# Optimization experiments

Hardware: AMD Instinct MI355X
Metric: run time of the kernel (lower is better)

## Reference

```python
import jax, jax.numpy as jnp
import numpy as np

N_GENE = 4762
N_CELL = 847


def _graph_conv(x_src, src, dst, n_src, n_dst, W, b):
    """DGL GraphConv with norm='both': D_src^{-1/2} A D_dst^{-1/2} X W + b."""
    ones_e = jnp.ones(src.shape, jnp.float32)
    deg_out = jax.ops.segment_sum(ones_e, src, num_segments=n_src)
    norm_src = jnp.clip(deg_out, 1.0, None) ** -0.5
    feat = x_src * norm_src[:, None]            # [n_src, d]
    msg = feat[src]                              # gather  [E, d]
    agg = jax.ops.segment_sum(msg, dst, num_segments=n_dst)  # scatter-add [n_dst, d]
    deg_in = jax.ops.segment_sum(ones_e, dst, num_segments=n_dst)
    norm_dst = jnp.clip(deg_in, 1.0, None) ** -0.5
    return (agg * norm_dst[:, None]) @ W + b


def setup_inputs() -> dict:
    key = jax.random.key(0)
    ks = jax.random.split(key, 12)
    E = 200000
    d = 256
    inp = {
        "gene_emb": jax.random.normal(ks[0], (N_GENE, d), jnp.float32),
        "cell_emb": jax.random.normal(ks[1], (N_CELL, d), jnp.float32),
        "W_g2c": jax.random.normal(ks[2], (d, d), jnp.float32) * (1.0 / np.sqrt(d)),
        "b_g2c": jnp.zeros((d,), jnp.float32),
        "W_c2g": jax.random.normal(ks[3], (d, d), jnp.float32) * (1.0 / np.sqrt(d)),
        "b_c2g": jnp.zeros((d,), jnp.float32),
        "Wp": jax.random.normal(ks[4], (2 * d, 1), jnp.float32) * (1.0 / np.sqrt(2 * d)),
        "bp": jnp.zeros((1,), jnp.float32),
        "g2c_src": jax.random.randint(ks[5], (E,), 0, N_GENE, jnp.int32),
        "g2c_dst": jax.random.randint(ks[6], (E,), 0, N_CELL, jnp.int32),
        "c2g_src": jax.random.randint(ks[7], (E,), 0, N_CELL, jnp.int32),
        "c2g_dst": jax.random.randint(ks[8], (E,), 0, N_GENE, jnp.int32),
        "dec_src": jax.random.randint(ks[9], (E,), 0, N_GENE, jnp.int32),
        "dec_dst": jax.random.randint(ks[10], (E,), 0, N_CELL, jnp.int32),
    }
    return inp


def reference(gene_emb, cell_emb, W_g2c, b_g2c, W_c2g, b_c2g, Wp, bp,
              g2c_src, g2c_dst, c2g_src, c2g_dst, dec_src, dec_dst):
    # HeteroGraphConv (aggregate='sum'): each dst type receives from one relation here.
    h_cell = _graph_conv(gene_emb, g2c_src, g2c_dst, N_GENE, N_CELL, W_g2c, b_g2c)
    h_gene = _graph_conv(cell_emb, c2g_src, c2g_dst, N_CELL, N_GENE, W_c2g, b_c2g)
    h_gene = jax.nn.relu(h_gene)
    h_cell = jax.nn.relu(h_cell)
    # HeteroMLPPredictor: concat(src_h, dst_h) @ Wp + bp on dec_graph edges.
    x = jnp.concatenate([h_gene[dec_src], h_cell[dec_dst]], axis=1)  # [E_dec, 512]
    score = x @ Wp + bp                                               # [E_dec, 1]
    return (score, h_gene, h_cell)
```

## Files before the change

### kernel.cpp

```cpp
#include <hip/hip_runtime.h>

#define N_GENE 4762
#define N_CELL 847
#define NEDGE  200000
#define D      256
#define NPART  64

typedef __attribute__((ext_vector_type(8))) short short8;
typedef __attribute__((ext_vector_type(8))) unsigned short ushort8v;
typedef __attribute__((ext_vector_type(4))) float f32x4;

#define S_G_OUT 0
#define S_C_IN  (S_G_OUT + N_GENE)
#define S_C_OUT (S_C_IN + N_CELL)
#define S_G_IN  (S_C_OUT + N_CELL)
#define NBINS   (S_G_IN + N_GENE)

#define ALIGN8(x) (((x) + 7) & ~7)

#define A_DEG      0
#define A_NRM      (A_DEG + NBINS)
#define A_OFFS_C   (A_NRM + NBINS)
#define A_OFFS_G   (A_OFFS_C + N_CELL + 1)
#define A_SORT_C   ALIGN8(A_OFFS_G + N_GENE + 1)
#define A_SORT_G   (A_SORT_C + 2 * NEDGE)
#define A_PART     (A_SORT_G + 2 * NEDGE)
#define A_SG       (A_PART + NPART * NBINS)
#define A_SC       (A_SG + N_GENE)
#define A_GENE_BF  ALIGN8(A_SC + N_CELL)
#define A_CELL_BF  ALIGN8(A_GENE_BF + N_GENE * D / 2)
#define A_WT1_BF   ALIGN8(A_CELL_BF + N_CELL * D / 2)
#define A_WT2_BF   ALIGN8(A_WT1_BF + D * D / 2)
#define A_AGGC_BF  ALIGN8(A_WT2_BF + D * D / 2)
#define A_AGGG_BF  ALIGN8(A_AGGC_BF + N_CELL * D / 2)

__device__ __forceinline__ unsigned short f2bf(float f) {
    unsigned u = __float_as_uint(f);
    u = (u + 0x7FFFu + ((u >> 16) & 1u)) >> 16;
    return (unsigned short)u;
}
__device__ __forceinline__ float bf2f(unsigned short b) {
    return __uint_as_float(((unsigned)b) << 16);
}

__global__ __launch_bounds__(1024) void k_pre(
        const int* __restrict__ g2c_src, const int* __restrict__ g2c_dst,
        const int* __restrict__ c2g_src, const int* __restrict__ c2g_dst,
        const float* __restrict__ gene_emb, const float* __restrict__ cell_emb,
        const float* __restrict__ W_g2c, const float* __restrict__ W_c2g,
        int* __restrict__ partial,
        unsigned short* __restrict__ gene_bf, unsigned short* __restrict__ cell_bf,
        unsigned short* __restrict__ wt1, unsigned short* __restrict__ wt2,
        float* __restrict__ sg, float* __restrict__ sc) {
    __shared__ int sh[N_GENE];
    int B = blockIdx.x, T = threadIdx.x;
    if (B < 4 * NPART) {
        int grp = B >> 6, blk = B & (NPART - 1);
        const int* idx;
        int segbase, segn;
        if      (grp == 0) { idx = g2c_src; segbase = S_G_OUT; segn = N_GENE; }
        else if (grp == 1) { idx = g2c_dst; segbase = S_C_IN;  segn = N_CELL; }
        else if (grp == 2) { idx = c2g_src; segbase = S_C_OUT; segn = N_CELL; }
        else               { idx = c2g_dst; segbase = S_G_IN;  segn = N_GENE; }
        for (int j = T; j < segn; j += 1024) sh[j] = 0;
        __syncthreads();
        const int chunk = (NEDGE + NPART - 1) / NPART;
        int e0 = blk * chunk, e1 = min(NEDGE, e0 + chunk);
        for (int e = e0 + T; e < e1; e += 1024) atomicAdd(&sh[idx[e]], 1);
        __syncthreads();
        int* pp = partial + blk * NBINS + segbase;
        for (int j = T; j < segn; j += 1024) pp[j] = sh[j];
    } else {
        const int NG = N_GENE * D, NC = N_CELL * D, NW = D * D;
        int base = (B - 4 * NPART) * 1024 + T;
        const int CH = (NG + NC) / 8;
        for (int c = base; c < CH; c += 64 * 1024) {
            const float* sp;
            unsigned short* dp;
            if (c < NG / 8) { sp = gene_emb + c * 8; dp = gene_bf + c * 8; }
            else { int j = (c - NG / 8) * 8; sp = cell_emb + j; dp = cell_bf + j; }
            f32x4 x0 = *(const f32x4*)sp;
            f32x4 x1 = *(const f32x4*)(sp + 4);
            ushort8v o;
            o[0] = f2bf(x0[0]); o[1] = f2bf(x0[1]);
            o[2] = f2bf(x0[2]); o[3] = f2bf(x0[3]);
            o[4] = f2bf(x1[0]); o[5] = f2bf(x1[1]);
            o[6] = f2bf(x1[2]); o[7] = f2bf(x1[3]);
            *(ushort8v*)dp = o;
        }
        for (int i = base; i < 2 * NW; i += 64 * 1024) {
            if (i < NW) {
                wt1[i] = f2bf(W_g2c[(i & 255) * D + (i >> 8)]);
            } else {
                int j = i - NW;
                wt2[j] = f2bf(W_c2g[(j & 255) * D + (j >> 8)]);
            }
        }
        for (int i = base; i < N_GENE + N_CELL; i += 64 * 1024) {
            if (i < N_GENE) sg[i] = 0.f; else sc[i - N_GENE] = 0.f;
        }
    }
}

__global__ void k_reduce(int* __restrict__ partial, int* __restrict__ deg,
                         float* __restrict__ nrm) {
    int j = blockIdx.x * blockDim.x + threadIdx.x;
    if (j < NBINS) {
        int s = 0;
        #pragma unroll
        for (int b0 = 0; b0 < NPART; b0 += 32) {
            int t[32];
            #pragma unroll
            for (int u = 0; u < 32; u++) t[u] = partial[(b0 + u) * NBINS + j];
            #pragma unroll
            for (int u = 0; u < 32; u++) { partial[(b0 + u) * NBINS + j] = s; s += t[u]; }
        }
        deg[j] = s;
        nrm[j] = rsqrtf(fmaxf((float)s, 1.0f));
    }
}

__global__ __launch_bounds__(1024) void k_scatter(
        const int* __restrict__ g2c_src, const int* __restrict__ g2c_dst,
        const int* __restrict__ c2g_src, const int* __restrict__ c2g_dst,
        const int* __restrict__ deg, const int* __restrict__ partial,
        const float* __restrict__ nrm,
        int* __restrict__ offsC, int* __restrict__ offsG,
        int2* __restrict__ sortC, int2* __restrict__ sortG) {
    __shared__ int soffs[N_GENE + 1];
    __shared__ int scur[N_GENE];
    __shared__ int wsum[16];
    int T = threadIdx.x, blk = blockIdx.x, dir = blockIdx.y;
    const int* src  = dir ? c2g_src : g2c_src;
    const int* dst  = dir ? c2g_dst : g2c_dst;
    const int* dgs  = dir ? deg + S_G_IN : deg + S_C_IN;
    const float* nsv = dir ? nrm + S_C_OUT : nrm + S_G_OUT;
    int seg         = dir ? S_G_IN : S_C_IN;
    int nb          = dir ? N_GENE : N_CELL;
    int* goffs      = dir ? offsG : offsC;
    int2* sorted    = dir ? sortG : sortC;
    int per = (nb + 1023) >> 10;
    int i0 = T * per, i1 = min(nb, i0 + per);
    int loc[5];
    int s = 0;
    for (int i = i0; i < i1; i++) { loc[i - i0] = s; s += dgs[i]; }
    int lane = T & 63, w = T >> 6;
    int t = s;
    #pragma unroll
    for (int off = 1; off < 64; off <<= 1) {
        int u = __shfl_up(t, off);
        if (lane >= off) t += u;
    }
    if (lane == 63) wsum[w] = t;
    __syncthreads();
    if (w == 0 && lane < 16) {
        int x = wsum[lane];
        #pragma unroll
        for (int off = 1; off < 16; off <<= 1) {
            int u = __shfl_up(x, off);
            if (lane >= off) x += u;
        }
        wsum[lane] = x;
    }
    __syncthreads();
    int wbase = w ? wsum[w - 1] : 0;
    int excl = wbase + t - s;
    for (int i = i0; i < i1; i++) soffs[i] = excl + loc[i - i0];
    if (T == 1023) soffs[nb] = excl + s;
    __syncthreads();
    if (blk == 0)
        for (int j = T; j <= nb; j += 1024) goffs[j] = soffs[j];
    const int* basep = partial + blk * NBINS + seg;
    for (int j = T; j < nb; j += 1024) scur[j] = soffs[j] + basep[j];
    __syncthreads();
    const int chunk = (NEDGE + NPART - 1) / NPART;
    int e0 = blk * chunk, e1 = min(NEDGE, e0 + chunk);
    for (int e = e0 + T; e < e1; e += 1024) {
        int d = dst[e], sv = src[e];
        float nv = nsv[sv];
        int pos = atomicAdd(&scur[d], 1);
        sorted[pos] = make_int2(sv, __float_as_int(nv));
    }
}

__global__ __launch_bounds__(256) void k_agg(
        const unsigned short* __restrict__ gene_bf,
        const unsigned short* __restrict__ cell_bf,
        const int2* __restrict__ sortC, const int2* __restrict__ sortG,
        const int* __restrict__ offsC, const int* __restrict__ offsG,
        const float* __restrict__ nrm,
        unsigned short* __restrict__ aggC, unsigned short* __restrict__ aggG) {
    __shared__ int   sidx[4][64];
    __shared__ float snrm[4][64];
    const int CB = (N_CELL + 3) / 4;
    int w = threadIdx.x >> 6, lane = threadIdx.x & 63;
    int half = lane >> 5, li = lane & 31;
    int B = blockIdx.x;
    bool isCell = B < CB;

    int e0, e1, node;
    const unsigned short* emb;
    const int2* sorted;
    unsigned short* outp;
    int nseg;
    if (isCell) {
        node = B * 4 + w;
        if (node >= N_CELL) return;
        e0 = offsC[node]; e1 = offsC[node + 1];
        emb = gene_bf; sorted = sortC; outp = aggC; nseg = S_C_IN;
    } else {
        node = (B - CB) * 4 + w;
        if (node >= N_GENE) return;
        e0 = offsG[node]; e1 = offsG[node + 1];
        emb = cell_bf; sorted = sortG; outp = aggG; nseg = S_G_IN;
    }

    float acc[8];
    #pragma unroll
    for (int c = 0; c < 8; c++) acc[c] = 0.f;

    for (int base = e0; base < e1; base += 64) {
        int n = min(64, e1 - base);
        if (lane < n) {
            int2 pr = sorted[base + lane];
            sidx[w][lane] = pr.x;
            snrm[w][lane] = __int_as_float(pr.y);
        }
        int i = 0;
        for (; 2 * i + 32 <= n; i += 16) {
            ushort8v v[16];
            float nv[16];
            #pragma unroll
            for (int k = 0; k < 16; k++) {
                int jj = 2 * (i + k) + half;
                v[k] = *(const ushort8v*)&emb[sidx[w][jj] * D + li * 8];
                nv[k] = snrm[w][jj];
            }
            #pragma unroll
            for (int c = 0; c < 8; c++) {
                float s0 = 0.f;
                #pragma unroll
                for (int k = 0; k < 16; k++) s0 += bf2f(v[k][c]) * nv[k];
                acc[c] += s0;
            }
        }
        for (; 2 * i + 16 <= n; i += 8) {
            ushort8v v[8];
            float nv[8];
            #pragma unroll
            for (int k = 0; k < 8; k++) {
                int jj = 2 * (i + k) + half;
                v[k] = *(const ushort8v*)&emb[sidx[w][jj] * D + li * 8];
                nv[k] = snrm[w][jj];
            }
            #pragma unroll
            for (int c = 0; c < 8; c++) {
                float s0 = 0.f;
                #pragma unroll
                for (int k = 0; k < 8; k++) s0 += bf2f(v[k][c]) * nv[k];
                acc[c] += s0;
            }
        }
        for (; 2 * i + 8 <= n; i += 4) {
            int j0 = 2 * i + half, j1 = 2 * i + 2 + half;
            int j2 = 2 * i + 4 + half, j3 = 2 * i + 6 + half;
            ushort8v v0 = *(const ushort8v*)&emb[sidx[w][j0] * D + li * 8];
            ushort8v v1 = *(const ushort8v*)&emb[sidx[w][j1] * D + li * 8];
            ushort8v v2 = *(const ushort8v*)&emb[sidx[w][j2] * D + li * 8];
            ushort8v v3 = *(const ushort8v*)&emb[sidx[w][j3] * D + li * 8];
            float n0 = snrm[w][j0], n1 = snrm[w][j1];
            float n2 = snrm[w][j2], n3 = snrm[w][j3];
            #pragma unroll
            for (int c = 0; c < 8; c++)
                acc[c] += bf2f(v0[c]) * n0 + bf2f(v1[c]) * n1 +
                          bf2f(v2[c]) * n2 + bf2f(v3[c]) * n3;
        }
        int npair = (n + 1) >> 1;
        for (; i < npair; i++) {
            int jj = 2 * i + half;
            bool ok = jj < n;
            int idx = ok ? sidx[w][jj] : sidx[w][0];
            float nv = ok ? snrm[w][jj] : 0.f;
            ushort8v v = *(const ushort8v*)&emb[idx * D + li * 8];
            #pragma unroll
            for (int c = 0; c < 8; c++) acc[c] += bf2f(v[c]) * nv;
        }
    }
    #pragma unroll
    for (int c = 0; c < 8; c++) acc[c] += __shfl_xor(acc[c], 32);

    if (half == 0) {
        float ndv = nrm[nseg + node];
        ushort8v o;
        #pragma unroll
        for (int c = 0; c < 8; c++) o[c] = f2bf(acc[c] * ndv);
        *(ushort8v*)&outp[node * D + li * 8] = o;
    }
}

__global__ __launch_bounds__(256) void k_gemm2(
        const unsigned short* __restrict__ aggC, const unsigned short* __restrict__ aggG,
        const unsigned short* __restrict__ wt1, const unsigned short* __restrict__ wt2,
        const float* __restrict__ b_g2c, const float* __restrict__ b_c2g,
        const float* __restrict__ Wp,
        float* __restrict__ hC, float* __restrict__ hG,
        float* __restrict__ sg, float* __restrict__ sc) {
    const int CT = (N_CELL + 15) / 16;
    const int GT = (N_GENE + 15) / 16;
    int wid = blockIdx.x * 4 + (threadIdx.x >> 6);
    if (wid >= (CT + GT) * 4) return;
    int tid = wid >> 2, nq = wid & 3;
    int n0 = nq * 64;
    bool isCell = tid < CT;
    int tile = isCell ? tid : tid - CT;
    int m0 = tile * 16;
    int M = isCell ? N_CELL : N_GENE;
    const unsigned short* A  = isCell ? aggC : aggG;
    const unsigned short* Wt = isCell ? wt1 : wt2;
    const float* bias = isCell ? b_g2c : b_c2g;
    const float* wp   = isCell ? Wp + D : Wp;
    float* H  = isCell ? hC : hG;
    float* sv = isCell ? sc : sg;
    int lane = threadIdx.x & 63;
    int l15 = lane & 15, quad = lane >> 4;
    int arow = m0 + l15;
    if (arow >= M) arow = M - 1;
    f32x4 acc[4];
    #pragma unroll
    for (int t = 0; t < 4; t++) acc[t] = (f32x4){0.f, 0.f, 0.f, 0.f};
    #pragma unroll
    for (int k0 = 0; k0 < D; k0 += 32) {
        short8 a = *(const short8*)&A[arow * D + k0 + quad * 8];
        #pragma unroll
        for (int t = 0; t < 4; t++) {
            short8 b = *(const short8*)&Wt[(n0 + t * 16 + l15) * D + k0 + quad * 8];
            acc[t] = __builtin_amdgcn_mfma_f32_16x16x32_bf16(a, b, acc[t], 0, 0, 0);
        }
    }
    float dot[4] = {0.f, 0.f, 0.f, 0.f};
    #pragma unroll
    for (int t = 0; t < 4; t++) {
        int col = n0 + t * 16 + l15;
        float bv = bias[col], wv = wp[col];
        #pragma unroll
        for (int r = 0; r < 4; r++) {
            int row = m0 + quad * 4 + r;
            float h = fmaxf(acc[t][r] + bv, 0.f);
            if (row < M) H[row * D + col] = h;
            dot[r] += h * wv;
        }
    }
    #pragma unroll
    for (int off = 1; off < 16; off <<= 1) {
        #pragma unroll
        for (int r = 0; r < 4; r++) dot[r] += __shfl_xor(dot[r], off);
    }
    if (l15 == 0) {
        #pragma unroll
        for (int r = 0; r < 4; r++) {
            int row = m0 + quad * 4 + r;
            if (row < M) atomicAdd(&sv[row], dot[r]);
        }
    }
}

__global__ void k_score(const int* __restrict__ dsrc, const int* __restrict__ ddst,
                        const float* __restrict__ sg, const float* __restrict__ sc,
                        const float* __restrict__ bp, float* __restrict__ out) {
    int i = blockIdx.x * blockDim.x + threadIdx.x;
    if (i < NEDGE) out[i] = sg[dsrc[i]] + sc[ddst[i]] + bp[0];
}

extern "C" void kernel_launch(void* const* d_in, const int* in_sizes, int n_in,
                              void* d_out, int out_size, void* d_ws, size_t ws_size,
                              hipStream_t stream) {
    const float* gene_emb = (const float*)d_in[0];
    const float* cell_emb = (const float*)d_in[1];
    const float* W_g2c    = (const float*)d_in[2];
    const float* b_g2c    = (const float*)d_in[3];
    const float* W_c2g    = (const float*)d_in[4];
    const float* b_c2g    = (const float*)d_in[5];
    const float* Wp       = (const float*)d_in[6];
    const float* bp       = (const float*)d_in[7];
    const int* g2c_src = (const int*)d_in[8];
    const int* g2c_dst = (const int*)d_in[9];
    const int* c2g_src = (const int*)d_in[10];
    const int* c2g_dst = (const int*)d_in[11];
    const int* dec_src = (const int*)d_in[12];
    const int* dec_dst = (const int*)d_in[13];

    int*   wsi = (int*)d_ws;
    float* wsf = (float*)d_ws;
    unsigned short* gene_bf = (unsigned short*)(wsi + A_GENE_BF);
    unsigned short* cell_bf = (unsigned short*)(wsi + A_CELL_BF);
    unsigned short* wt1     = (unsigned short*)(wsi + A_WT1_BF);
    unsigned short* wt2     = (unsigned short*)(wsi + A_WT2_BF);
    unsigned short* aggC    = (unsigned short*)(wsi + A_AGGC_BF);
    unsigned short* aggG    = (unsigned short*)(wsi + A_AGGG_BF);
    int2* sortC = (int2*)(wsi + A_SORT_C);
    int2* sortG = (int2*)(wsi + A_SORT_G);

    float* out = (float*)d_out;
    float* out_score = out;
    float* out_hgene = out + NEDGE;
    float* out_hcell = out + NEDGE + N_GENE * D;

    k_pre<<<4 * NPART + 64, 1024, 0, stream>>>(g2c_src, g2c_dst, c2g_src, c2g_dst,
                                               gene_emb, cell_emb, W_g2c, W_c2g,
                                               wsi + A_PART, gene_bf, cell_bf, wt1, wt2,
                                               wsf + A_SG, wsf + A_SC);
    k_reduce<<<(NBINS + 255) / 256, 256, 0, stream>>>(wsi + A_PART, wsi + A_DEG,
                                                      wsf + A_NRM);
    {
        dim3 grid(NPART, 2);
        k_scatter<<<grid, 1024, 0, stream>>>(g2c_src, g2c_dst, c2g_src, c2g_dst,
                                             wsi + A_DEG, wsi + A_PART, wsf + A_NRM,
                                             wsi + A_OFFS_C, wsi + A_OFFS_G,
                                             sortC, sortG);
    }
    {
        const int CB = (N_CELL + 3) / 4, GB = (N_GENE + 3) / 4;
        k_agg<<<CB + GB, 256, 0, stream>>>(
            gene_bf, cell_bf, sortC, sortG, wsi + A_OFFS_C, wsi + A_OFFS_G,
            wsf + A_NRM, aggC, aggG);
    }
    {
        const int CT = (N_CELL + 15) / 16, GT = (N_GENE + 15) / 16;
        k_gemm2<<<CT + GT, 256, 0, stream>>>(aggC, aggG, wt1, wt2,
                                             b_g2c, b_c2g, Wp,
                                             out_hcell, out_hgene,
                                             wsf + A_SG, wsf + A_SC);
    }
    k_score<<<(NEDGE + 255) / 256, 256, 0, stream>>>(dec_src, dec_dst,
                                                     wsf + A_SG, wsf + A_SC, bp, out_score);
}
```

Baseline: 141.4 us.

## Split cell aggregation into fixed edge chunks with atomic fp32 accumulation

Cell-destination aggregation used one wave per cell. With about 236 edges per cell that gave few, long waves, so the work was poorly balanced. It now splits the sorted edge list into 128-edge chunks, one per wave. Each wave binary-searches the CSR offsets to find its starting cell and atomically adds partial sums into an fp32 buffer, which k_pre zeroes. The aggregate buffers become fp32, and the destination-norm scaling plus bf16 conversion move into the GEMM's A-load. This adds atomic traffic and doubles the size of the intermediate buffers.

```diff
diff --git a/kernel.cpp b/kernel.cpp
--- a/kernel.cpp
+++ b/kernel.cpp
@@ -5,6 +5,7 @@
 #define NEDGE  200000
 #define D      256
 #define NPART  64
+#define CCHUNK 128
 
 typedef __attribute__((ext_vector_type(8))) short short8;
 typedef __attribute__((ext_vector_type(8))) unsigned short ushort8v;
@@ -31,8 +32,8 @@
 #define A_CELL_BF  ALIGN8(A_GENE_BF + N_GENE * D / 2)
 #define A_WT1_BF   ALIGN8(A_CELL_BF + N_CELL * D / 2)
 #define A_WT2_BF   ALIGN8(A_WT1_BF + D * D / 2)
-#define A_AGGC_BF  ALIGN8(A_WT2_BF + D * D / 2)
-#define A_AGGG_BF  ALIGN8(A_AGGC_BF + N_CELL * D / 2)
+#define A_AGGC_F   ALIGN8(A_WT2_BF + D * D / 2)
+#define A_AGGG_F   (A_AGGC_F + N_CELL * D)
 
 __device__ __forceinline__ unsigned short f2bf(float f) {
     unsigned u = __float_as_uint(f);
@@ -51,7 +52,8 @@
         int* __restrict__ partial,
         unsigned short* __restrict__ gene_bf, unsigned short* __restrict__ cell_bf,
         unsigned short* __restrict__ wt1, unsigned short* __restrict__ wt2,
-        float* __restrict__ sg, float* __restrict__ sc) {
+        float* __restrict__ sg, float* __restrict__ sc,
+        float* __restrict__ aggCf) {
     __shared__ int sh[N_GENE];
     int B = blockIdx.x, T = threadIdx.x;
     if (B < 4 * NPART) {
@@ -99,6 +101,9 @@
         for (int i = base; i < N_GENE + N_CELL; i += 64 * 1024) {
             if (i < N_GENE) sg[i] = 0.f; else sc[i - N_GENE] = 0.f;
         }
+        f32x4 z = {0.f, 0.f, 0.f, 0.f};
+        for (int i = base; i < N_CELL * D / 4; i += 64 * 1024)
+            ((f32x4*)aggCf)[i] = z;
     }
 }
 
@@ -183,126 +188,149 @@
     }
 }
 
+__device__ __forceinline__ void gather_acc(
+        const unsigned short* __restrict__ emb,
+        const int2* __restrict__ sorted,
+        int* __restrict__ sidxw, float* __restrict__ snrmw,
+        int lane, int half, int li, int rs, int re, float acc[8]) {
+    for (int base = rs; base < re; base += 64) {
+        int n = min(64, re - base);
+        if (lane < n) {
+            int2 pr = sorted[base + lane];
+            sidxw[lane] = pr.x;
+            snrmw[lane] = __int_as_float(pr.y);
+        }
+        int i = 0;
+        for (; 2 * i + 32 <= n; i += 16) {
+            ushort8v v[16];
+            float nv[16];
+            #pragma unroll
+            for (int k = 0; k < 16; k++) {
+                int jj = 2 * (i + k) + half;
+                v[k] = *(const ushort8v*)&emb[sidxw[jj] * D + li * 8];
+                nv[k] = snrmw[jj];
+            }
+            #pragma unroll
+            for (int c = 0; c < 8; c++) {
+                float s0 = 0.f;
+                #pragma unroll
+                for (int k = 0; k < 16; k++) s0 += bf2f(v[k][c]) * nv[k];
+                acc[c] += s0;
+            }
+        }
+        for (; 2 * i + 16 <= n; i += 8) {
+            ushort8v v[8];
+            float nv[8];
+            #pragma unroll
+            for (int k = 0; k < 8; k++) {
+                int jj = 2 * (i + k) + half;
+                v[k] = *(const ushort8v*)&emb[sidxw[jj] * D + li * 8];
+                nv[k] = snrmw[jj];
+            }
+            #pragma unroll
+            for (int c = 0; c < 8; c++) {
+                float s0 = 0.f;
+                #pragma unroll
+                for (int k = 0; k < 8; k++) s0 += bf2f(v[k][c]) * nv[k];
+                acc[c] += s0;
+            }
+        }
+        for (; 2 * i + 8 <= n; i += 4) {
+            int j0 = 2 * i + half, j1 = 2 * i + 2 + half;
+            int j2 = 2 * i + 4 + half, j3 = 2 * i + 6 + half;
+            ushort8v v0 = *(const ushort8v*)&emb[sidxw[j0] * D + li * 8];
+            ushort8v v1 = *(const ushort8v*)&emb[sidxw[j1] * D + li * 8];
+            ushort8v v2 = *(const ushort8v*)&emb[sidxw[j2] * D + li * 8];
+            ushort8v v3 = *(const ushort8v*)&emb[sidxw[j3] * D + li * 8];
+            float n0 = snrmw[j0], n1 = snrmw[j1];
+            float n2 = snrmw[j2], n3 = snrmw[j3];
+            #pragma unroll
+            for (int c = 0; c < 8; c++)
+                acc[c] += bf2f(v0[c]) * n0 + bf2f(v1[c]) * n1 +
+                          bf2f(v2[c]) * n2 + bf2f(v3[c]) * n3;
+        }
+        int npair = (n + 1) >> 1;
+        for (; i < npair; i++) {
+            int jj = 2 * i + half;
+            bool ok = jj < n;
+            int idx = ok ? sidxw[jj] : sidxw[0];
+            float nv = ok ? snrmw[jj] : 0.f;
+            ushort8v v = *(const ushort8v*)&emb[idx * D + li * 8];
+            #pragma unroll
+            for (int c = 0; c < 8; c++) acc[c] += bf2f(v[c]) * nv;
+        }
+    }
+}
+
 __global__ __launch_bounds__(256) void k_agg(
         const unsigned short* __restrict__ gene_bf,
         const unsigned short* __restrict__ cell_bf,
         const int2* __restrict__ sortC, const int2* __restrict__ sortG,
         const int* __restrict__ offsC, const int* __restrict__ offsG,
-        const float* __restrict__ nrm,
-        unsigned short* __restrict__ aggC, unsigned short* __restrict__ aggG) {
+        float* __restrict__ aggCf, float* __restrict__ aggGf) {
     __shared__ int   sidx[4][64];
     __shared__ float snrm[4][64];
-    const int CB = (N_CELL + 3) / 4;
+    const int NCH  = (NEDGE + CCHUNK - 1) / CCHUNK;
+    const int CBLK = (NCH + 3) / 4;
     int w = threadIdx.x >> 6, lane = threadIdx.x & 63;
     int half = lane >> 5, li = lane & 31;
     int B = blockIdx.x;
-    bool isCell = B < CB;
-
-    int e0, e1, node;
-    const unsigned short* emb;
-    const int2* sorted;
-    unsigned short* outp;
-    int nseg;
-    if (isCell) {
-        node = B * 4 + w;
-        if (node >= N_CELL) return;
-        e0 = offsC[node]; e1 = offsC[node + 1];
-        emb = gene_bf; sorted = sortC; outp = aggC; nseg = S_C_IN;
+
+    if (B < CBLK) {
+        int chunk = B * 4 + w;
+        if (chunk >= NCH) return;
+        int e0 = chunk * CCHUNK, e1 = min(NEDGE, e0 + CCHUNK);
+        int lo = 0, hi = N_CELL - 1;
+        while (lo < hi) {
+            int m = (lo + hi + 1) >> 1;
+            if (offsC[m] <= e0) lo = m; else hi = m - 1;
+        }
+        int d = lo, rs = e0;
+        while (rs < e1 && d < N_CELL) {
+            int re = min(e1, offsC[d + 1]);
+            if (re > rs) {
+                float acc[8];
+                #pragma unroll
+                for (int c = 0; c < 8; c++) acc[c] = 0.f;
+                gather_acc(gene_bf, sortC, sidx[w], snrm[w],
+                           lane, half, li, rs, re, acc);
+                #pragma unroll
+                for (int c = 0; c < 8; c++) acc[c] += __shfl_xor(acc[c], 32);
+                if (half == 0) {
+                    float* dstp = &aggCf[d * D + li * 8];
+                    #pragma unroll
+                    for (int c = 0; c < 8; c++) atomicAdd(&dstp[c], acc[c]);
+                }
+                rs = re;
+            }
+            d++;
+        }
     } else {
-        node = (B - CB) * 4 + w;
+        int node = (B - CBLK) * 4 + w;
         if (node >= N_GENE) return;
-        e0 = offsG[node]; e1 = offsG[node + 1];
-        emb = cell_bf; sorted = sortG; outp = aggG; nseg = S_G_IN;
-    }
-
-    float acc[8];
-    #pragma unroll
-    for (int c = 0; c < 8; c++) acc[c] = 0.f;
-
-    for (int base = e0; base < e1; base += 64) {
-        int n = min(64, e1 - base);
-        if (lane < n) {
-            int2 pr = sorted[base + lane];
-            sidx[w][lane] = pr.x;
-            snrm[w][lane] = __int_as_float(pr.y);
-        }
-        int i = 0;
-        for (; 2 * i + 32 <= n; i += 16) {
-            ushort8v v[16];
-            float nv[16];
-            #pragma unroll
-            for (int k = 0; k < 16; k++) {
-                int jj = 2 * (i + k) + half;
-                v[k] = *(const ushort8v*)&emb[sidx[w][jj] * D + li * 8];
-                nv[k] = snrm[w][jj];
-            }
-            #pragma unroll
-            for (int c = 0; c < 8; c++) {
-                float s0 = 0.f;
-                #pragma unroll
-                for (int k = 0; k < 16; k++) s0 += bf2f(v[k][c]) * nv[k];
-                acc[c] += s0;
-            }
-        }
-        for (; 2 * i + 16 <= n; i += 8) {
-            ushort8v v[8];
-            float nv[8];
-            #pragma unroll
-            for (int k = 0; k < 8; k++) {
-                int jj = 2 * (i + k) + half;
-                v[k] = *(const ushort8v*)&emb[sidx[w][jj] * D + li * 8];
-                nv[k] = snrm[w][jj];
-            }
-            #pragma unroll
-            for (int c = 0; c < 8; c++) {
-                float s0 = 0.f;
-                #pragma unroll
-                for (int k = 0; k < 8; k++) s0 += bf2f(v[k][c]) * nv[k];
-                acc[c] += s0;
-            }
-        }
-        for (; 2 * i + 8 <= n; i += 4) {
-            int j0 = 2 * i + half, j1 = 2 * i + 2 + half;
-            int j2 = 2 * i + 4 + half, j3 = 2 * i + 6 + half;
-            ushort8v v0 = *(const ushort8v*)&emb[sidx[w][j0] * D + li * 8];
-            ushort8v v1 = *(const ushort8v*)&emb[sidx[w][j1] * D + li * 8];
-            ushort8v v2 = *(const ushort8v*)&emb[sidx[w][j2] * D + li * 8];
-            ushort8v v3 = *(const ushort8v*)&emb[sidx[w][j3] * D + li * 8];
-            float n0 = snrm[w][j0], n1 = snrm[w][j1];
-            float n2 = snrm[w][j2], n3 = snrm[w][j3];
-            #pragma unroll
-            for (int c = 0; c < 8; c++)
-                acc[c] += bf2f(v0[c]) * n0 + bf2f(v1[c]) * n1 +
-                          bf2f(v2[c]) * n2 + bf2f(v3[c]) * n3;
-        }
-        int npair = (n + 1) >> 1;
-        for (; i < npair; i++) {
-            int jj = 2 * i + half;
-            bool ok = jj < n;
-            int idx = ok ? sidx[w][jj] : sidx[w][0];
-            float nv = ok ? snrm[w][jj] : 0.f;
-            ushort8v v = *(const ushort8v*)&emb[idx * D + li * 8];
-            #pragma unroll
-            for (int c = 0; c < 8; c++) acc[c] += bf2f(v[c]) * nv;
-        }
-    }
-    #pragma unroll
-    for (int c = 0; c < 8; c++) acc[c] += __shfl_xor(acc[c], 32);
-
-    if (half == 0) {
-        float ndv = nrm[nseg + node];
-        ushort8v o;
-        #pragma unroll
-        for (int c = 0; c < 8; c++) o[c] = f2bf(acc[c] * ndv);
-        *(ushort8v*)&outp[node * D + li * 8] = o;
+        int e0 = offsG[node], e1 = offsG[node + 1];
+        float acc[8];
+        #pragma unroll
+        for (int c = 0; c < 8; c++) acc[c] = 0.f;
+        gather_acc(cell_bf, sortG, sidx[w], snrm[w],
+                   lane, half, li, e0, e1, acc);
+        #pragma unroll
+        for (int c = 0; c < 8; c++) acc[c] += __shfl_xor(acc[c], 32);
+        if (half == 0) {
+            f32x4 o0, o1;
+            #pragma unroll
+            for (int c = 0; c < 4; c++) { o0[c] = acc[c]; o1[c] = acc[4 + c]; }
+            *(f32x4*)&aggGf[node * D + li * 8] = o0;
+            *(f32x4*)&aggGf[node * D + li * 8 + 4] = o1;
+        }
     }
 }
 
 __global__ __launch_bounds__(256) void k_gemm2(
-        const unsigned short* __restrict__ aggC, const unsigned short* __restrict__ aggG,
+        const float* __restrict__ aggCf, const float* __restrict__ aggGf,
         const unsigned short* __restrict__ wt1, const unsigned short* __restrict__ wt2,
         const float* __restrict__ b_g2c, const float* __restrict__ b_c2g,
-        const float* __restrict__ Wp,
+        const float* __restrict__ Wp, const float* __restrict__ nrm,
         float* __restrict__ hC, float* __restrict__ hG,
         float* __restrict__ sg, float* __restrict__ sc) {
     const int CT = (N_CELL + 15) / 16;
@@ -315,22 +343,31 @@
     int tile = isCell ? tid : tid - CT;
     int m0 = tile * 16;
     int M = isCell ? N_CELL : N_GENE;
-    const unsigned short* A  = isCell ? aggC : aggG;
+    const float* A = isCell ? aggCf : aggGf;
     const unsigned short* Wt = isCell ? wt1 : wt2;
     const float* bias = isCell ? b_g2c : b_c2g;
     const float* wp   = isCell ? Wp + D : Wp;
     float* H  = isCell ? hC : hG;
     float* sv = isCell ? sc : sg;
+    int nseg  = isCell ? S_C_IN : S_G_IN;
     int lane = threadIdx.x & 63;
     int l15 = lane & 15, quad = lane >> 4;
     int arow = m0 + l15;
     if (arow >= M) arow = M - 1;
+    float nrmv = nrm[nseg + arow];
     f32x4 acc[4];
     #pragma unroll
     for (int t = 0; t < 4; t++) acc[t] = (f32x4){0.f, 0.f, 0.f, 0.f};
     #pragma unroll
     for (int k0 = 0; k0 < D; k0 += 32) {
-        short8 a = *(const short8*)&A[arow * D + k0 + quad * 8];
+        f32x4 a0 = *(const f32x4*)&A[arow * D + k0 + quad * 8];
+        f32x4 a1 = *(const f32x4*)&A[arow * D + k0 + quad * 8 + 4];
+        short8 a;
+        #pragma unroll
+        for (int j = 0; j < 4; j++) {
+            a[j]     = (short)f2bf(a0[j] * nrmv);
+            a[4 + j] = (short)f2bf(a1[j] * nrmv);
+        }
         #pragma unroll
         for (int t = 0; t < 4; t++) {
             short8 b = *(const short8*)&Wt[(n0 + t * 16 + l15) * D + k0 + quad * 8];
@@ -395,8 +432,8 @@
     unsigned short* cell_bf = (unsigned short*)(wsi + A_CELL_BF);
     unsigned short* wt1     = (unsigned short*)(wsi + A_WT1_BF);
     unsigned short* wt2     = (unsigned short*)(wsi + A_WT2_BF);
-    unsigned short* aggC    = (unsigned short*)(wsi + A_AGGC_BF);
-    unsigned short* aggG    = (unsigned short*)(wsi + A_AGGG_BF);
+    float* aggCf = wsf + A_AGGC_F;
+    float* aggGf = wsf + A_AGGG_F;
     int2* sortC = (int2*)(wsi + A_SORT_C);
     int2* sortG = (int2*)(wsi + A_SORT_G);
 
@@ -408,7 +445,7 @@
     k_pre<<<4 * NPART + 64, 1024, 0, stream>>>(g2c_src, g2c_dst, c2g_src, c2g_dst,
                                                gene_emb, cell_emb, W_g2c, W_c2g,
                                                wsi + A_PART, gene_bf, cell_bf, wt1, wt2,
-                                               wsf + A_SG, wsf + A_SC);
+                                               wsf + A_SG, wsf + A_SC, aggCf);
     k_reduce<<<(NBINS + 255) / 256, 256, 0, stream>>>(wsi + A_PART, wsi + A_DEG,
                                                       wsf + A_NRM);
     {
@@ -419,15 +456,16 @@
                                              sortC, sortG);
     }
     {
-        const int CB = (N_CELL + 3) / 4, GB = (N_GENE + 3) / 4;
-        k_agg<<<CB + GB, 256, 0, stream>>>(
+        const int NCH = (NEDGE + CCHUNK - 1) / CCHUNK;
+        const int CBLK = (NCH + 3) / 4, GB = (N_GENE + 3) / 4;
+        k_agg<<<CBLK + GB, 256, 0, stream>>>(
             gene_bf, cell_bf, sortC, sortG, wsi + A_OFFS_C, wsi + A_OFFS_G,
-            wsf + A_NRM, aggC, aggG);
+            aggCf, aggGf);
     }
     {
         const int CT = (N_CELL + 15) / 16, GT = (N_GENE + 15) / 16;
-        k_gemm2<<<CT + GT, 256, 0, stream>>>(aggC, aggG, wt1, wt2,
-                                             b_g2c, b_c2g, Wp,
+        k_gemm2<<<CT + GT, 256, 0, stream>>>(aggCf, aggGf, wt1, wt2,
+                                             b_g2c, b_c2g, Wp, wsf + A_NRM,
                                              out_hcell, out_hgene,
                                              wsf + A_SG, wsf + A_SC);
     }
```

Measured after the change: 147.4 us. 1.04x slower.

## Fuse front-end and back-end kernels with inter-block flag synchronization

Applied to the files above, without the earlier changes.

Merges the histogram, prefix-reduce and scatter kernels into one launch, and the GEMM and score kernels into another. Dependent block groups spin-wait on per-block flags in workspace, set with release and acquire fences. This removes three kernel launches and their gaps. The flags are never reset, so on repeated calls they already hold the magic value and the waits fall through, which can race with stale data. The scheme also relies on producer blocks being resident before consumers spin.

```diff
diff --git a/kernel.cpp b/kernel.cpp
--- a/kernel.cpp
+++ b/kernel.cpp
@@ -5,6 +5,7 @@
 #define NEDGE  200000
 #define D      256
 #define NPART  64
+#define MAGIC  0x7A3B9C1D
 
 typedef __attribute__((ext_vector_type(8))) short short8;
 typedef __attribute__((ext_vector_type(8))) unsigned short ushort8v;
@@ -27,7 +28,8 @@
 #define A_PART     (A_SORT_G + 2 * NEDGE)
 #define A_SG       (A_PART + NPART * NBINS)
 #define A_SC       (A_SG + N_GENE)
-#define A_GENE_BF  ALIGN8(A_SC + N_CELL)
+#define A_FLAGS    ALIGN8(A_SC + N_CELL)
+#define A_GENE_BF  ALIGN8(A_FLAGS + 640)
 #define A_CELL_BF  ALIGN8(A_GENE_BF + N_GENE * D / 2)
 #define A_WT1_BF   ALIGN8(A_CELL_BF + N_CELL * D / 2)
 #define A_WT2_BF   ALIGN8(A_WT1_BF + D * D / 2)
@@ -43,17 +45,38 @@
     return __uint_as_float(((unsigned)b) << 16);
 }
 
-__global__ __launch_bounds__(1024) void k_pre(
+__device__ __forceinline__ void sig(int* slot) {
+    __builtin_amdgcn_fence(__ATOMIC_RELEASE, "agent");
+    __hip_atomic_store(slot, MAGIC, __ATOMIC_RELAXED, __HIP_MEMORY_SCOPE_AGENT);
+}
+__device__ __forceinline__ void waitflags(const int* slots, int n, int T, int nthr) {
+    for (int s = T; s < n; s += nthr) {
+        long long t0 = (long long)__builtin_amdgcn_s_memrealtime();
+        while (__hip_atomic_load(&slots[s], __ATOMIC_RELAXED,
+                                 __HIP_MEMORY_SCOPE_AGENT) != MAGIC) {
+            __builtin_amdgcn_s_sleep(2);
+            if ((long long)__builtin_amdgcn_s_memrealtime() - t0 > 50000000LL) break;
+        }
+    }
+    __syncthreads();
+    __builtin_amdgcn_fence(__ATOMIC_ACQUIRE, "agent");
+}
+
+__global__ __launch_bounds__(1024) void k_front(
         const int* __restrict__ g2c_src, const int* __restrict__ g2c_dst,
         const int* __restrict__ c2g_src, const int* __restrict__ c2g_dst,
         const float* __restrict__ gene_emb, const float* __restrict__ cell_emb,
         const float* __restrict__ W_g2c, const float* __restrict__ W_c2g,
-        int* __restrict__ partial,
+        int* __restrict__ partial, int* __restrict__ deg, float* __restrict__ nrm,
+        int* __restrict__ offsC, int* __restrict__ offsG,
+        int2* __restrict__ sortC, int2* __restrict__ sortG,
         unsigned short* __restrict__ gene_bf, unsigned short* __restrict__ cell_bf,
         unsigned short* __restrict__ wt1, unsigned short* __restrict__ wt2,
-        float* __restrict__ sg, float* __restrict__ sc) {
-    __shared__ int sh[N_GENE];
+        float* __restrict__ sg, float* __restrict__ sc,
+        int* __restrict__ flags) {
+    __shared__ int shm[2 * N_GENE + 24];
     int B = blockIdx.x, T = threadIdx.x;
+
     if (B < 4 * NPART) {
         int grp = B >> 6, blk = B & (NPART - 1);
         const int* idx;
@@ -62,15 +85,17 @@
         else if (grp == 1) { idx = g2c_dst; segbase = S_C_IN;  segn = N_CELL; }
         else if (grp == 2) { idx = c2g_src; segbase = S_C_OUT; segn = N_CELL; }
         else               { idx = c2g_dst; segbase = S_G_IN;  segn = N_GENE; }
-        for (int j = T; j < segn; j += 1024) sh[j] = 0;
+        for (int j = T; j < segn; j += 1024) shm[j] = 0;
         __syncthreads();
         const int chunk = (NEDGE + NPART - 1) / NPART;
         int e0 = blk * chunk, e1 = min(NEDGE, e0 + chunk);
-        for (int e = e0 + T; e < e1; e += 1024) atomicAdd(&sh[idx[e]], 1);
+        for (int e = e0 + T; e < e1; e += 1024) atomicAdd(&shm[idx[e]], 1);
         __syncthreads();
         int* pp = partial + blk * NBINS + segbase;
-        for (int j = T; j < segn; j += 1024) pp[j] = sh[j];
-    } else {
+        for (int j = T; j < segn; j += 1024) pp[j] = shm[j];
+        __syncthreads();
+        if (T == 0) sig(&flags[B]);
+    } else if (B < 4 * NPART + 64) {
         const int NG = N_GENE * D, NC = N_CELL * D, NW = D * D;
         int base = (B - 4 * NPART) * 1024 + T;
         const int CH = (NG + NC) / 8;
@@ -99,87 +124,81 @@
         for (int i = base; i < N_GENE + N_CELL; i += 64 * 1024) {
             if (i < N_GENE) sg[i] = 0.f; else sc[i - N_GENE] = 0.f;
         }
-    }
-}
-
-__global__ void k_reduce(int* __restrict__ partial, int* __restrict__ deg,
-                         float* __restrict__ nrm) {
-    int j = blockIdx.x * blockDim.x + threadIdx.x;
-    if (j < NBINS) {
+    } else if (B < 4 * NPART + 64 + 11) {
+        waitflags(flags, 256, T, 1024);
+        int j = (B - (4 * NPART + 64)) * 1024 + T;
+        if (j < NBINS) {
+            int s = 0;
+            #pragma unroll
+            for (int b0 = 0; b0 < NPART; b0 += 32) {
+                int t[32];
+                #pragma unroll
+                for (int u = 0; u < 32; u++) t[u] = partial[(b0 + u) * NBINS + j];
+                #pragma unroll
+                for (int u = 0; u < 32; u++) { partial[(b0 + u) * NBINS + j] = s; s += t[u]; }
+            }
+            deg[j] = s;
+            nrm[j] = rsqrtf(fmaxf((float)s, 1.0f));
+        }
+        __syncthreads();
+        if (T == 0) sig(&flags[256 + (B - (4 * NPART + 64))]);
+    } else {
+        waitflags(flags + 256, 11, T, 1024);
+        int idx2 = B - (4 * NPART + 64 + 11);
+        int blk = idx2 & (NPART - 1), dir = idx2 >> 6;
+        int* soffs = shm;
+        int* scur  = shm + N_GENE + 1;
+        int* wsum  = shm + 2 * N_GENE + 1;
+        const int* src  = dir ? c2g_src : g2c_src;
+        const int* dst  = dir ? c2g_dst : g2c_dst;
+        const int* dgs  = dir ? deg + S_G_IN : deg + S_C_IN;
+        const float* nsv = dir ? nrm + S_C_OUT : nrm + S_G_OUT;
+        int seg         = dir ? S_G_IN : S_C_IN;
+        int nb          = dir ? N_GENE : N_CELL;
+        int* goffs      = dir ? offsG : offsC;
+        int2* sorted    = dir ? sortG : sortC;
+        int per = (nb + 1023) >> 10;
+        int i0 = T * per, i1 = min(nb, i0 + per);
+        int loc[5];
         int s = 0;
-        #pragma unroll
-        for (int b0 = 0; b0 < NPART; b0 += 32) {
-            int t[32];
-            #pragma unroll
-            for (int u = 0; u < 32; u++) t[u] = partial[(b0 + u) * NBINS + j];
-            #pragma unroll
-            for (int u = 0; u < 32; u++) { partial[(b0 + u) * NBINS + j] = s; s += t[u]; }
-        }
-        deg[j] = s;
-        nrm[j] = rsqrtf(fmaxf((float)s, 1.0f));
-    }
-}
-
-__global__ __launch_bounds__(1024) void k_scatter(
-        const int* __restrict__ g2c_src, const int* __restrict__ g2c_dst,
-        const int* __restrict__ c2g_src, const int* __restrict__ c2g_dst,
-        const int* __restrict__ deg, const int* __restrict__ partial,
-        const float* __restrict__ nrm,
-        int* __restrict__ offsC, int* __restrict__ offsG,
-        int2* __restrict__ sortC, int2* __restrict__ sortG) {
-    __shared__ int soffs[N_GENE + 1];
-    __shared__ int scur[N_GENE];
-    __shared__ int wsum[16];
-    int T = threadIdx.x, blk = blockIdx.x, dir = blockIdx.y;
-    const int* src  = dir ? c2g_src : g2c_src;
-    const int* dst  = dir ? c2g_dst : g2c_dst;
-    const int* dgs  = dir ? deg + S_G_IN : deg + S_C_IN;
-    const float* nsv = dir ? nrm + S_C_OUT : nrm + S_G_OUT;
-    int seg         = dir ? S_G_IN : S_C_IN;
-    int nb          = dir ? N_GENE : N_CELL;
-    int* goffs      = dir ? offsG : offsC;
-    int2* sorted    = dir ? sortG : sortC;
-    int per = (nb + 1023) >> 10;
-    int i0 = T * per, i1 = min(nb, i0 + per);
-    int loc[5];
-    int s = 0;
-    for (int i = i0; i < i1; i++) { loc[i - i0] = s; s += dgs[i]; }
-    int lane = T & 63, w = T >> 6;
-    int t = s;
-    #pragma unroll
-    for (int off = 1; off < 64; off <<= 1) {
-        int u = __shfl_up(t, off);
-        if (lane >= off) t += u;
-    }
-    if (lane == 63) wsum[w] = t;
-    __syncthreads();
-    if (w == 0 && lane < 16) {
-        int x = wsum[lane];
-        #pragma unroll
-        for (int off = 1; off < 16; off <<= 1) {
-            int u = __shfl_up(x, off);
-            if (lane >= off) x += u;
-        }
-        wsum[lane] = x;
-    }
-    __syncthreads();
-    int wbase = w ? wsum[w - 1] : 0;
-    int excl = wbase + t - s;
-    for (int i = i0; i < i1; i++) soffs[i] = excl + loc[i - i0];
-    if (T == 1023) soffs[nb] = excl + s;
-    __syncthreads();
-    if (blk == 0)
-        for (int j = T; j <= nb; j += 1024) goffs[j] = soffs[j];
-    const int* basep = partial + blk * NBINS + seg;
-    for (int j = T; j < nb; j += 1024) scur[j] = soffs[j] + basep[j];
-    __syncthreads();
-    const int chunk = (NEDGE + NPART - 1) / NPART;
-    int e0 = blk * chunk, e1 = min(NEDGE, e0 + chunk);
-    for (int e = e0 + T; e < e1; e += 1024) {
-        int d = dst[e], sv = src[e];
-        float nv = nsv[sv];
-        int pos = atomicAdd(&scur[d], 1);
-        sorted[pos] = make_int2(sv, __float_as_int(nv));
+        for (int i = i0; i < i1; i++) { loc[i - i0] = s; s += dgs[i]; }
+        int lane = T & 63, w = T >> 6;
+        int t = s;
+        #pragma unroll
+        for (int off = 1; off < 64; off <<= 1) {
+            int u = __shfl_up(t, off);
+            if (lane >= off) t += u;
+        }
+        if (lane == 63) wsum[w] = t;
+        __syncthreads();
+        if (w == 0 && lane < 16) {
+            int x = wsum[lane];
+            #pragma unroll
+            for (int off = 1; off < 16; off <<= 1) {
+                int u = __shfl_up(x, off);
+                if (lane >= off) x += u;
+            }
+            wsum[lane] = x;
+        }
+        __syncthreads();
+        int wbase = w ? wsum[w - 1] : 0;
+        int excl = wbase + t - s;
+        for (int i = i0; i < i1; i++) soffs[i] = excl + loc[i - i0];
+        if (T == 1023) soffs[nb] = excl + s;
+        __syncthreads();
+        if (blk == 0)
+            for (int j = T; j <= nb; j += 1024) goffs[j] = soffs[j];
+        const int* basep = partial + blk * NBINS + seg;
+        for (int j = T; j < nb; j += 1024) scur[j] = soffs[j] + basep[j];
+        __syncthreads();
+        const int chunk = (NEDGE + NPART - 1) / NPART;
+        int e0 = blk * chunk, e1 = min(NEDGE, e0 + chunk);
+        for (int e = e0 + T; e < e1; e += 1024) {
+            int d = dst[e], sv = src[e];
+            float nv = nsv[sv];
+            int pos = atomicAdd(&scur[d], 1);
+            sorted[pos] = make_int2(sv, __float_as_int(nv));
+        }
     }
 }
 
@@ -298,77 +317,83 @@
     }
 }
 
-__global__ __launch_bounds__(256) void k_gemm2(
+__global__ __launch_bounds__(256) void k_back(
         const unsigned short* __restrict__ aggC, const unsigned short* __restrict__ aggG,
         const unsigned short* __restrict__ wt1, const unsigned short* __restrict__ wt2,
         const float* __restrict__ b_g2c, const float* __restrict__ b_c2g,
         const float* __restrict__ Wp,
         float* __restrict__ hC, float* __restrict__ hG,
-        float* __restrict__ sg, float* __restrict__ sc) {
+        float* __restrict__ sg, float* __restrict__ sc,
+        const int* __restrict__ dsrc, const int* __restrict__ ddst,
+        const float* __restrict__ bp, float* __restrict__ out,
+        int* __restrict__ flags) {
     const int CT = (N_CELL + 15) / 16;
     const int GT = (N_GENE + 15) / 16;
-    int wid = blockIdx.x * 4 + (threadIdx.x >> 6);
-    if (wid >= (CT + GT) * 4) return;
-    int tid = wid >> 2, nq = wid & 3;
-    int n0 = nq * 64;
-    bool isCell = tid < CT;
-    int tile = isCell ? tid : tid - CT;
-    int m0 = tile * 16;
-    int M = isCell ? N_CELL : N_GENE;
-    const unsigned short* A  = isCell ? aggC : aggG;
-    const unsigned short* Wt = isCell ? wt1 : wt2;
-    const float* bias = isCell ? b_g2c : b_c2g;
-    const float* wp   = isCell ? Wp + D : Wp;
-    float* H  = isCell ? hC : hG;
-    float* sv = isCell ? sc : sg;
-    int lane = threadIdx.x & 63;
-    int l15 = lane & 15, quad = lane >> 4;
-    int arow = m0 + l15;
-    if (arow >= M) arow = M - 1;
-    f32x4 acc[4];
-    #pragma unroll
-    for (int t = 0; t < 4; t++) acc[t] = (f32x4){0.f, 0.f, 0.f, 0.f};
-    #pragma unroll
-    for (int k0 = 0; k0 < D; k0 += 32) {
-        short8 a = *(const short8*)&A[arow * D + k0 + quad * 8];
+    int B = blockIdx.x, T = threadIdx.x;
+    if (B < CT + GT) {
+        int wid = B * 4 + (T >> 6);
+        int tid = wid >> 2, nq = wid & 3;
+        int n0 = nq * 64;
+        bool isCell = tid < CT;
+        int tile = isCell ? tid : tid - CT;
+        int m0 = tile * 16;
+        int M = isCell ? N_CELL : N_GENE;
+        const unsigned short* A  = isCell ? aggC : aggG;
+        const unsigned short* Wt = isCell ? wt1 : wt2;
+        const float* bias = isCell ? b_g2c : b_c2g;
+        const float* wp   = isCell ? Wp + D : Wp;
+        float* H  = isCell ? hC : hG;
+        float* sv = isCell ? sc : sg;
+        int lane = T & 63;
+        int l15 = lane & 15, quad = lane >> 4;
+        int arow = m0 + l15;
+        if (arow >= M) arow = M - 1;
+        f32x4 acc[4];
+        #pragma unroll
+        for (int t = 0; t < 4; t++) acc[t] = (f32x4){0.f, 0.f, 0.f, 0.f};
+        #pragma unroll
+        for (int k0 = 0; k0 < D; k0 += 32) {
+            short8 a = *(const short8*)&A[arow * D + k0 + quad * 8];
+            #pragma unroll
+            for (int t = 0; t < 4; t++) {
+                short8 b = *(const short8*)&Wt[(n0 + t * 16 + l15) * D + k0 + quad * 8];
+                acc[t] = __builtin_amdgcn_mfma_f32_16x16x32_bf16(a, b, acc[t], 0, 0, 0);
+            }
+        }
+        float dot[4] = {0.f, 0.f, 0.f, 0.f};
         #pragma unroll
         for (int t = 0; t < 4; t++) {
-            short8 b = *(const short8*)&Wt[(n0 + t * 16 + l15) * D + k0 + quad * 8];
-            acc[t] = __builtin_amdgcn_mfma_f32_16x16x32_bf16(a, b, acc[t], 0, 0, 0);
-        }
-    }
-    float dot[4] = {0.f, 0.f, 0.f, 0.f};
-    #pragma unroll
-    for (int t = 0; t < 4; t++) {
-        int col = n0 + t * 16 + l15;
-        float bv = bias[col], wv = wp[col];
-        #pragma unroll
-        for (int r = 0; r < 4; r++) {
-            int row = m0 + quad * 4 + r;
-            float h = fmaxf(acc[t][r] + bv, 0.f);
-            if (row < M) H[row * D + col] = h;
-            dot[r] += h * wv;
-        }
-    }
-    #pragma unroll
-    for (int off = 1; off < 16; off <<= 1) {
-        #pragma unroll
-        for (int r = 0; r < 4; r++) dot[r] += __shfl_xor(dot[r], off);
-    }
-    if (l15 == 0) {
-        #pragma unroll
-        for (int r = 0; r < 4; r++) {
-            int row = m0 + quad * 4 + r;
-            if (row < M) atomicAdd(&sv[row], dot[r]);
-        }
-    }
-}
-
-__global__ void k_score(const int* __restrict__ dsrc, const int* __restrict__ ddst,
-                        const float* __restrict__ sg, const float* __restrict__ sc,
-                        const float* __restrict__ bp, float* __restrict__ out) {
-    int i = blockIdx.x * blockDim.x + threadIdx.x;
-    if (i < NEDGE) out[i] = sg[dsrc[i]] + sc[ddst[i]] + bp[0];
+            int col = n0 + t * 16 + l15;
+            float bv = bias[col], wv = wp[col];
+            #pragma unroll
+            for (int r = 0; r < 4; r++) {
+                int row = m0 + quad * 4 + r;
+                float h = fmaxf(acc[t][r] + bv, 0.f);
+                if (row < M) H[row * D + col] = h;
+                dot[r] += h * wv;
+            }
+        }
+        #pragma unroll
+        for (int off = 1; off < 16; off <<= 1) {
+            #pragma unroll
+            for (int r = 0; r < 4; r++) dot[r] += __shfl_xor(dot[r], off);
+        }
+        if (l15 == 0) {
+            #pragma unroll
+            for (int r = 0; r < 4; r++) {
+                int row = m0 + quad * 4 + r;
+                if (row < M) atomicAdd(&sv[row], dot[r]);
+            }
+        }
+        __syncthreads();
+        if (T == 0) sig(&flags[267 + B]);
+    } else {
+        waitflags(flags + 267, CT + GT, T, 256);
+        float bpv = bp[0];
+        int i0 = (B - (CT + GT)) * 256 + T;
+        for (int i = i0; i < NEDGE; i += 128 * 256)
+            out[i] = sg[dsrc[i]] + sc[ddst[i]] + bpv;
+    }
 }
 
 extern "C" void kernel_launch(void* const* d_in, const int* in_sizes, int n_in,
@@ -405,19 +430,12 @@
     float* out_hgene = out + NEDGE;
     float* out_hcell = out + NEDGE + N_GENE * D;
 
-    k_pre<<<4 * NPART + 64, 1024, 0, stream>>>(g2c_src, g2c_dst, c2g_src, c2g_dst,
-                                               gene_emb, cell_emb, W_g2c, W_c2g,
-                                               wsi + A_PART, gene_bf, cell_bf, wt1, wt2,
-                                               wsf + A_SG, wsf + A_SC);
-    k_reduce<<<(NBINS + 255) / 256, 256, 0, stream>>>(wsi + A_PART, wsi + A_DEG,
-                                                      wsf + A_NRM);
-    {
-        dim3 grid(NPART, 2);
-        k_scatter<<<grid, 1024, 0, stream>>>(g2c_src, g2c_dst, c2g_src, c2g_dst,
-                                             wsi + A_DEG, wsi + A_PART, wsf + A_NRM,
-                                             wsi + A_OFFS_C, wsi + A_OFFS_G,
-                                             sortC, sortG);
-    }
+    k_front<<<4 * NPART + 64 + 11 + 2 * NPART, 1024, 0, stream>>>(
+        g2c_src, g2c_dst, c2g_src, c2g_dst, gene_emb, cell_emb, W_g2c, W_c2g,
+        wsi + A_PART, wsi + A_DEG, wsf + A_NRM,
+        wsi + A_OFFS_C, wsi + A_OFFS_G, sortC, sortG,
+        gene_bf, cell_bf, wt1, wt2, wsf + A_SG, wsf + A_SC,
+        wsi + A_FLAGS);
     {
         const int CB = (N_CELL + 3) / 4, GB = (N_GENE + 3) / 4;
         k_agg<<<CB + GB, 256, 0, stream>>>(
@@ -426,11 +444,9 @@
     }
     {
         const int CT = (N_CELL + 15) / 16, GT = (N_GENE + 15) / 16;
-        k_gemm2<<<CT + GT, 256, 0, stream>>>(aggC, aggG, wt1, wt2,
-                                             b_g2c, b_c2g, Wp,
-                                             out_hcell, out_hgene,
-                                             wsf + A_SG, wsf + A_SC);
-    }
-    k_score<<<(NEDGE + 255) / 256, 256, 0, stream>>>(dec_src, dec_dst,
-                                                     wsf + A_SG, wsf + A_SC, bp, out_score);
-}
+        k_back<<<CT + GT + 128, 256, 0, stream>>>(
+            aggC, aggG, wt1, wt2, b_g2c, b_c2g, Wp,
+            out_hcell, out_hgene, wsf + A_SG, wsf + A_SC,
+            dec_src, dec_dst, bp, out_score, wsi + A_FLAGS);
+    }
+}
```

Result: slower. 179.5 us (+27.0%).
